# Kernel tuning notes

Hardware: AMD Instinct MI355X
Metric: run time of the kernel (lower is better)

The kernel has to match this reference:

```python
import jax, jax.numpy as jnp
import numpy as np


def setup_inputs() -> dict:
    key = jax.random.key(0)
    ks = jax.random.split(key, 4)
    T, B, E = 2048, 2, 1024
    query = jax.random.normal(ks[0], (T, B, E), dtype=jnp.float32)
    attn_mask = jnp.zeros((T, T), dtype=jnp.float32)
    Wqkv = jax.random.normal(ks[1], (3 * E, E), dtype=jnp.float32) * 0.02
    bqkv = jnp.zeros((3 * E,), dtype=jnp.float32)
    Wout = jax.random.normal(ks[2], (E, E), dtype=jnp.float32) * 0.02
    bout = jnp.zeros((E,), dtype=jnp.float32)
    return {"query": query, "attn_mask": attn_mask, "Wqkv": Wqkv,
            "bqkv": bqkv, "Wout": Wout, "bout": bout, "num_heads": 16}


def reference(query, attn_mask, Wqkv, bqkv, Wout, bout, num_heads):
    T, B, E = query.shape
    H = num_heads
    hd = E // H
    scaling = hd ** -0.5
    # fused QKV projection: [T,B,3E]
    qkv = jnp.einsum('tbe,fe->tbf', query, Wqkv) + bqkv
    q, k, v = jnp.split(qkv, 3, axis=-1)
    q = q * scaling
    # [T,B,E] -> [B*H, T, hd]
    def to_heads(x):
        return x.reshape(T, B * H, hd).transpose(1, 0, 2)
    q, k, v = to_heads(q), to_heads(k), to_heads(v)
    # scores [B*H, T, T]
    scores = jnp.einsum('bth,bsh->bts', q, k) + attn_mask[None, :, :]
    probs = jax.nn.softmax(scores, axis=-1)  # dropout p=0
    attn = jnp.einsum('bts,bsh->bth', probs, v)  # [B*H, T, hd]
    attn = attn.transpose(1, 0, 2).reshape(T, B, E)
    out = jnp.einsum('tbe,fe->tbf', attn, Wout) + bout
    avg_w = probs.reshape(B, H, T, T).sum(axis=1) / H
    return out, avg_w
```

## Files before the change

kernel.cpp:

```cpp
#include <hip/hip_runtime.h>
#include <cstdint>
#include <cstddef>

#define Tt 2048
#define Bb 2
#define Ee 1024
#define Hh 16
#define HD 64
#define BHh (Bb*Hh)
#define Mm (Tt*Bb)

typedef short bf16x8 __attribute__((ext_vector_type(8)));
typedef float f32x4  __attribute__((ext_vector_type(4)));

#define MFMA16(a,b,c) __builtin_amdgcn_mfma_f32_16x16x32_bf16(a, b, c, 0, 0, 0)

__device__ __forceinline__ unsigned short f2bf(float f) {
    unsigned int u = __builtin_bit_cast(unsigned int, f);
    u += 0x7FFFu + ((u >> 16) & 1u);
    return (unsigned short)(u >> 16);
}
__device__ __forceinline__ unsigned int pack2bf(float lo, float hi) {
    return (unsigned int)f2bf(lo) | ((unsigned int)f2bf(hi) << 16);
}

__device__ __forceinline__ bf16x8 ldfrag(const unsigned short* base, int row, int col) {
    const unsigned int* p = (const unsigned int*)(base + row*66 + col);
    const unsigned int* q = (const unsigned int*)(base + row*66 + col + 16);
    uint4 u;
    u.x = p[0]; u.y = p[1];
    u.z = q[0]; u.w = q[1];
    return __builtin_bit_cast(bf16x8, u);
}

__global__ __launch_bounds__(256)
void to_bf16(const float* __restrict__ src, unsigned short* __restrict__ dst, int n8)
{
    const int stride = gridDim.x * 256;
    for (int i = blockIdx.x*256 + threadIdx.x; i < n8; i += stride) {
        const float4 a = ((const float4*)src)[2*i];
        const float4 b = ((const float4*)src)[2*i + 1];
        const uint4 u = {pack2bf(a.x,a.y), pack2bf(a.z,a.w),
                         pack2bf(b.x,b.y), pack2bf(b.z,b.w)};
        ((uint4*)dst)[i] = u;
    }
}

template<int MODE>
__global__ __launch_bounds__(256)
void gemm_mfma(const unsigned short* __restrict__ A, const unsigned short* __restrict__ W,
               const float* __restrict__ bias, float* __restrict__ Cout,
               unsigned short* __restrict__ qbuf, unsigned short* __restrict__ kbuf,
               unsigned short* __restrict__ vbuf, int N, int K)
{
    __shared__ unsigned short As[128][66];
    __shared__ unsigned short Ws[128][66];
    const int tid  = threadIdx.x;
    const int bm   = blockIdx.y * 128;
    const int bn   = blockIdx.x * 128;
    const int w    = tid >> 6;
    const int lane = tid & 63;
    const int lr   = lane & 15;
    const int lg   = lane >> 4;
    const int wm   = (w >> 1) * 64;
    const int wn   = (w & 1) * 64;

    f32x4 acc[4][4];
#pragma unroll
    for (int m = 0; m < 4; ++m)
#pragma unroll
        for (int n = 0; n < 4; ++n)
            acc[m][n] = f32x4{0.f, 0.f, 0.f, 0.f};

    const int sr = tid >> 1;
    const int sc = (tid & 1) * 16;

    for (int k0 = 0; k0 < K; k0 += 32) {
        __syncthreads();
        {
            const unsigned short* Ap = &A[(size_t)(bm + sr) * K + k0 + sc];
            const unsigned short* Wp = &W[(size_t)(bn + sr) * K + k0 + sc];
            const uint4 a0 = *(const uint4*)Ap;
            const uint4 a1 = *(const uint4*)(Ap + 8);
            const uint4 w0 = *(const uint4*)Wp;
            const uint4 w1 = *(const uint4*)(Wp + 8);
            *(uint4*)&As[sr][sc]     = a0;
            *(uint4*)&As[sr][sc + 8] = a1;
            *(uint4*)&Ws[sr][sc]     = w0;
            *(uint4*)&Ws[sr][sc + 8] = w1;
        }
        __syncthreads();

        bf16x8 af[4], wf[4];
#pragma unroll
        for (int i = 0; i < 4; ++i) {
            af[i] = ldfrag(&As[0][0], wm + 16*i + lr, 4*lg);
            wf[i] = ldfrag(&Ws[0][0], wn + 16*i + lr, 4*lg);
        }
#pragma unroll
        for (int m = 0; m < 4; ++m)
#pragma unroll
            for (int n = 0; n < 4; ++n)
                acc[m][n] = MFMA16(af[m], wf[n], acc[m][n]);
    }

#pragma unroll
    for (int nsub = 0; nsub < 4; ++nsub) {
        const int n0 = bn + wn + 16*nsub + lr;
        const float bv = bias[n0];
#pragma unroll
        for (int msub = 0; msub < 4; ++msub) {
#pragma unroll
            for (int reg = 0; reg < 4; ++reg) {
                const int m = bm + wm + 16*msub + 4*lg + reg;
                float v = acc[msub][nsub][reg] + bv;
                if (MODE == 0) {
                    const int which = n0 >> 10;
                    const int e0 = n0 & 1023;
                    const int h = e0 >> 6, d0 = e0 & 63;
                    if (which == 0) v *= 0.125f;
                    unsigned short* dst = (which == 0) ? qbuf : (which == 1) ? kbuf : vbuf;
                    dst[((size_t)((m & 1)*Hh + h) * Tt + (m >> 1)) * HD + d0] = f2bf(v);
                } else {
                    Cout[(size_t)m * N + n0] = v;
                }
            }
        }
    }
}

__global__ __launch_bounds__(512)
void attn_mfma(const unsigned short* __restrict__ qb, const unsigned short* __restrict__ kb,
               const unsigned short* __restrict__ vb, const float* __restrict__ mask,
               unsigned short* __restrict__ attnb, float* __restrict__ lbuf)
{
    __shared__ unsigned short Ks[64][66];
    __shared__ unsigned short Vt[64][66];
    __shared__ float l_sh[128];

    const int tid  = threadIdx.x;
    const int bid  = blockIdx.x;
    const int wid  = (bid & 7) * 64 + (bid >> 3);
    const int bh   = wid & 31;
    const int t0   = (wid >> 5) * 128;
    const int w    = tid >> 6;
    const int lane = tid & 63;
    const int lr   = lane & 15;
    const int lg   = lane >> 4;
    const int b = bh >> 4, h = bh & 15;

    const unsigned short* __restrict__ Qg = qb + (size_t)bh * Tt * HD;
    const unsigned short* __restrict__ Kg = kb + (size_t)bh * Tt * HD;
    const unsigned short* __restrict__ Vg = vb + (size_t)bh * Tt * HD;

    const int str = tid >> 3;
    const int stc = (tid & 7) * 8;

    bf16x8 qf[2];
    for (int half = 0; half < 2; ++half) {
        __syncthreads();
        *(uint4*)&Ks[str][stc] =
            *(const uint4*)&Qg[(size_t)(t0 + half*64 + str) * HD + stc];
        __syncthreads();
        if ((w >> 2) == half) {
            const int r = 16*(w & 3) + lr;
            qf[0] = ldfrag(&Ks[0][0], r, 4*lg);
            qf[1] = ldfrag(&Ks[0][0], r, 32 + 4*lg);
        }
    }

    f32x4 oacc[4];
#pragma unroll
    for (int d = 0; d < 4; ++d)
        oacc[d] = f32x4{0.f, 0.f, 0.f, 0.f};
    float lacc = 0.f;

    for (int s0 = 0; s0 < Tt; s0 += 64) {
        __syncthreads();
        *(uint4*)&Ks[str][stc] =
            *(const uint4*)&Kg[(size_t)(s0 + str) * HD + stc];
        {
            const int dg = tid & 15, s2 = tid >> 4;
            const uint2 a = *(const uint2*)&Vg[(size_t)(s0 + 2*s2)     * HD + dg*4];
            const uint2 c = *(const uint2*)&Vg[(size_t)(s0 + 2*s2 + 1) * HD + dg*4];
            *(unsigned int*)&Vt[dg*4+0][2*s2] = (a.x & 0xFFFFu) | (c.x << 16);
            *(unsigned int*)&Vt[dg*4+1][2*s2] = (a.x >> 16)     | (c.x & 0xFFFF0000u);
            *(unsigned int*)&Vt[dg*4+2][2*s2] = (a.y & 0xFFFFu) | (c.y << 16);
            *(unsigned int*)&Vt[dg*4+3][2*s2] = (a.y >> 16)     | (c.y & 0xFFFF0000u);
        }
        __syncthreads();

        f32x4 sacc[4];
#pragma unroll
        for (int ssub = 0; ssub < 4; ++ssub) {
            const bf16x8 a0 = ldfrag(&Ks[0][0], 16*ssub + lr, 4*lg);
            const bf16x8 a1 = ldfrag(&Ks[0][0], 16*ssub + lr, 32 + 4*lg);
            f32x4 z = {0.f, 0.f, 0.f, 0.f};
            z = MFMA16(a0, qf[0], z);
            z = MFMA16(a1, qf[1], z);
            sacc[ssub] = z;
        }

        unsigned int pw[8];
        {
            float lt = 0.f;
            const float* __restrict__ mrow =
                &mask[(size_t)(t0 + 16*w + lr) * Tt + s0];
#pragma unroll
            for (int ssub = 0; ssub < 4; ++ssub) {
                const float4 mv = *(const float4*)&mrow[16*ssub + 4*lg];
                const float e0 = __expf(sacc[ssub][0] + mv.x);
                const float e1 = __expf(sacc[ssub][1] + mv.y);
                const float e2 = __expf(sacc[ssub][2] + mv.z);
                const float e3 = __expf(sacc[ssub][3] + mv.w);
                lt += (e0 + e1) + (e2 + e3);
                pw[ssub*2]     = pack2bf(e0, e1);
                pw[ssub*2 + 1] = pack2bf(e2, e3);
            }
            lt += __shfl_xor(lt, 16);
            lt += __shfl_xor(lt, 32);
            lacc += lt;
        }

        const uint4 ua = {pw[0], pw[1], pw[2], pw[3]};
        const uint4 ub = {pw[4], pw[5], pw[6], pw[7]};
#pragma unroll
        for (int dsub = 0; dsub < 4; ++dsub) {
            const bf16x8 b0 = ldfrag(&Vt[0][0], 16*dsub + lr, 4*lg);
            const bf16x8 b1 = ldfrag(&Vt[0][0], 16*dsub + lr, 32 + 4*lg);
            oacc[dsub] = MFMA16(__builtin_bit_cast(bf16x8, ua), b0, oacc[dsub]);
            oacc[dsub] = MFMA16(__builtin_bit_cast(bf16x8, ub), b1, oacc[dsub]);
        }
    }

    __syncthreads();
    if (lg == 0) l_sh[16*w + lr] = lacc;
    __syncthreads();
#pragma unroll
    for (int reg = 0; reg < 4; ++reg) {
        const int tl = 16*w + 4*lg + reg;
        const float inv = 1.f / l_sh[tl];
        const int t = t0 + tl;
#pragma unroll
        for (int dsub = 0; dsub < 4; ++dsub)
            attnb[((size_t)t * Bb + b) * Ee + h*HD + dsub*16 + lr] =
                f2bf(oacc[dsub][reg] * inv);
    }
    if (lg == 0)
        lbuf[(size_t)bh * Tt + t0 + 16*w + lr] = lacc;
}

__global__ __launch_bounds__(256)
void avg_probs_mfma(const unsigned short* __restrict__ qb, const unsigned short* __restrict__ kb,
                    const float* __restrict__ mask, const float* __restrict__ lbuf,
                    float* __restrict__ avg)
{
    __shared__ unsigned short Qs[64][66];
    __shared__ unsigned short Ksh[64][66];
    __shared__ float linv[16][64];

    const int tid  = threadIdx.x;
    const int b    = blockIdx.z;
    const int t0   = blockIdx.y * 64;
    const int s0   = blockIdx.x * 64;
    const int w    = tid >> 6;
    const int lane = tid & 63;
    const int lr   = lane & 15;
    const int lg   = lane >> 4;

    {
        const int h = tid >> 4, tl = (tid & 15) * 4;
        const float4 lv = *(const float4*)&lbuf[(size_t)(b*Hh + h) * Tt + t0 + tl];
        linv[h][tl+0] = 1.f / (16.f * lv.x);
        linv[h][tl+1] = 1.f / (16.f * lv.y);
        linv[h][tl+2] = 1.f / (16.f * lv.z);
        linv[h][tl+3] = 1.f / (16.f * lv.w);
    }

    f32x4 mf[4];
#pragma unroll
    for (int ssub = 0; ssub < 4; ++ssub)
#pragma unroll
        for (int reg = 0; reg < 4; ++reg)
            mf[ssub][reg] = mask[(size_t)(t0 + 16*w + 4*lg + reg) * Tt + s0 + 16*ssub + lr];

    f32x4 av[4];
#pragma unroll
    for (int ssub = 0; ssub < 4; ++ssub) av[ssub] = f32x4{0.f, 0.f, 0.f, 0.f};

    const int str = tid >> 2;
    const int stc = (tid & 3) * 16;

    for (int h = 0; h < Hh; ++h) {
        const unsigned short* __restrict__ Qg = qb + (size_t)(b*Hh + h) * Tt * HD;
        const unsigned short* __restrict__ Kg = kb + (size_t)(b*Hh + h) * Tt * HD;
        __syncthreads();
        {
            const unsigned short* Qp = &Qg[(size_t)(t0 + str) * HD + stc];
            const unsigned short* Kp = &Kg[(size_t)(s0 + str) * HD + stc];
            const uint4 q0 = *(const uint4*)Qp;
            const uint4 q1 = *(const uint4*)(Qp + 8);
            const uint4 k0 = *(const uint4*)Kp;
            const uint4 k1 = *(const uint4*)(Kp + 8);
            *(uint4*)&Qs[str][stc]      = q0;
            *(uint4*)&Qs[str][stc + 8]  = q1;
            *(uint4*)&Ksh[str][stc]     = k0;
            *(uint4*)&Ksh[str][stc + 8] = k1;
        }
        __syncthreads();

        const float lv0 = linv[h][16*w + 4*lg + 0];
        const float lv1 = linv[h][16*w + 4*lg + 1];
        const float lv2 = linv[h][16*w + 4*lg + 2];
        const float lv3 = linv[h][16*w + 4*lg + 3];

        const bf16x8 af0 = ldfrag(&Qs[0][0], 16*w + lr, 4*lg);
        const bf16x8 af1 = ldfrag(&Qs[0][0], 16*w + lr, 32 + 4*lg);
#pragma unroll
        for (int ssub = 0; ssub < 4; ++ssub) {
            const bf16x8 bf0 = ldfrag(&Ksh[0][0], 16*ssub + lr, 4*lg);
            const bf16x8 bf1 = ldfrag(&Ksh[0][0], 16*ssub + lr, 32 + 4*lg);
            f32x4 z = {0.f, 0.f, 0.f, 0.f};
            z = MFMA16(af0, bf0, z);
            z = MFMA16(af1, bf1, z);
            av[ssub][0] += __expf(z[0] + mf[ssub][0]) * lv0;
            av[ssub][1] += __expf(z[1] + mf[ssub][1]) * lv1;
            av[ssub][2] += __expf(z[2] + mf[ssub][2]) * lv2;
            av[ssub][3] += __expf(z[3] + mf[ssub][3]) * lv3;
        }
    }

#pragma unroll
    for (int ssub = 0; ssub < 4; ++ssub)
#pragma unroll
        for (int reg = 0; reg < 4; ++reg)
            avg[((size_t)b * Tt + t0 + 16*w + 4*lg + reg) * Tt + s0 + 16*ssub + lr] =
                av[ssub][reg];
}

extern "C" void kernel_launch(void* const* d_in, const int* in_sizes, int n_in,
                              void* d_out, int out_size, void* d_ws, size_t ws_size,
                              hipStream_t stream)
{
    (void)in_sizes; (void)n_in; (void)out_size; (void)ws_size;
    const float* query = (const float*)d_in[0];
    const float* mask  = (const float*)d_in[1];
    const float* Wqkv  = (const float*)d_in[2];
    const float* bqkv  = (const float*)d_in[3];
    const float* Wout  = (const float*)d_in[4];
    const float* bout  = (const float*)d_in[5];

    float* out = (float*)d_out;
    float* avg = out + (size_t)Tt * Bb * Ee;

    const size_t S1 = (size_t)BHh * Tt * HD;
    unsigned short* wsu     = (unsigned short*)d_ws;
    unsigned short* qbuf    = wsu;
    unsigned short* kbuf    = qbuf + S1;
    unsigned short* vbuf    = kbuf + S1;
    unsigned short* attnb   = vbuf + S1;
    unsigned short* querybf = attnb + (size_t)Mm * Ee;
    unsigned short* wqkvbf  = querybf + (size_t)Mm * Ee;
    unsigned short* woutbf  = wqkvbf + (size_t)3 * Ee * Ee;
    float*          lbuf    = (float*)(woutbf + (size_t)Ee * Ee);

    to_bf16<<<1024, 256, 0, stream>>>(query, querybf, (Mm*Ee)/8);
    to_bf16<<<1024, 256, 0, stream>>>(Wqkv, wqkvbf, (3*Ee*Ee)/8);
    to_bf16<<<512,  256, 0, stream>>>(Wout, woutbf, (Ee*Ee)/8);

    gemm_mfma<0><<<dim3(3072/128, Mm/128), 256, 0, stream>>>(
        querybf, wqkvbf, bqkv, nullptr, qbuf, kbuf, vbuf, 3072, Ee);
    attn_mfma<<<dim3(BHh * (Tt/128)), 512, 0, stream>>>(
        qbuf, kbuf, vbuf, mask, attnb, lbuf);
    avg_probs_mfma<<<dim3(Tt/64, Tt/64, Bb), 256, 0, stream>>>(
        qbuf, kbuf, mask, lbuf, avg);
    gemm_mfma<1><<<dim3(Ee/128, Mm/128), 256, 0, stream>>>(
        attnb, woutbf, bout, out, nullptr, nullptr, nullptr, Ee, Ee);
}
```

Baseline: 244.3 us.

## Use XOR-swizzled LDS layouts with 128-bit fragment loads in GEMM and attention

Replaces the padded (stride-66) shared-memory tiles with unpadded dword arrays indexed through XOR swizzles, in both the projection GEMM and the attention kernel. Fragments are now read with single 128-bit LDS loads instead of four 32-bit loads. The V transpose store is remapped with a permuted column index so the MFMA k-ordering stays consistent between the P and V operands. The aim is fewer LDS instructions and fewer bank conflicts, at the cost of trickier indexing that must keep the QK and PV contraction orderings matched.

```diff
diff --git a/kernel.cpp b/kernel.cpp
--- a/kernel.cpp
+++ b/kernel.cpp
@@ -24,6 +24,13 @@
     return (unsigned int)f2bf(lo) | ((unsigned int)f2bf(hi) << 16);
 }
 
+__device__ __forceinline__ int swzA(int row, int dwcol) {
+    return (row*32 + dwcol) ^ ((row & 7) << 2);
+}
+__device__ __forceinline__ int swzG(int row, int dwcol) {
+    return (row*16 + dwcol) ^ ((row & 3) << 2);
+}
+
 __device__ __forceinline__ bf16x8 ldfrag(const unsigned short* base, int row, int col) {
     const unsigned int* p = (const unsigned int*)(base + row*66 + col);
     const unsigned int* q = (const unsigned int*)(base + row*66 + col + 16);
@@ -53,8 +60,8 @@
                unsigned short* __restrict__ qbuf, unsigned short* __restrict__ kbuf,
                unsigned short* __restrict__ vbuf, int N, int K)
 {
-    __shared__ unsigned short As[128][66];
-    __shared__ unsigned short Ws[128][66];
+    __shared__ __align__(16) unsigned int AsDW[128*16];
+    __shared__ __align__(16) unsigned int WsDW[128*16];
     const int tid  = threadIdx.x;
     const int bm   = blockIdx.y * 128;
     const int bn   = blockIdx.x * 128;
@@ -72,30 +79,28 @@
         for (int n = 0; n < 4; ++n)
             acc[m][n] = f32x4{0.f, 0.f, 0.f, 0.f};
 
-    const int sr = tid >> 1;
-    const int sc = (tid & 1) * 16;
+    const int r1  = tid >> 2;
+    const int cdw = (tid & 3) * 4;
 
     for (int k0 = 0; k0 < K; k0 += 32) {
         __syncthreads();
         {
-            const unsigned short* Ap = &A[(size_t)(bm + sr) * K + k0 + sc];
-            const unsigned short* Wp = &W[(size_t)(bn + sr) * K + k0 + sc];
-            const uint4 a0 = *(const uint4*)Ap;
-            const uint4 a1 = *(const uint4*)(Ap + 8);
-            const uint4 w0 = *(const uint4*)Wp;
-            const uint4 w1 = *(const uint4*)(Wp + 8);
-            *(uint4*)&As[sr][sc]     = a0;
-            *(uint4*)&As[sr][sc + 8] = a1;
-            *(uint4*)&Ws[sr][sc]     = w0;
-            *(uint4*)&Ws[sr][sc + 8] = w1;
+            const uint4 a0 = *(const uint4*)&A[(size_t)(bm + r1)      * K + k0 + cdw*2];
+            const uint4 a1 = *(const uint4*)&A[(size_t)(bm + r1 + 64) * K + k0 + cdw*2];
+            const uint4 w0 = *(const uint4*)&W[(size_t)(bn + r1)      * K + k0 + cdw*2];
+            const uint4 w1 = *(const uint4*)&W[(size_t)(bn + r1 + 64) * K + k0 + cdw*2];
+            *(uint4*)(AsDW + swzG(r1,      cdw)) = a0;
+            *(uint4*)(AsDW + swzG(r1 + 64, cdw)) = a1;
+            *(uint4*)(WsDW + swzG(r1,      cdw)) = w0;
+            *(uint4*)(WsDW + swzG(r1 + 64, cdw)) = w1;
         }
         __syncthreads();
 
         bf16x8 af[4], wf[4];
 #pragma unroll
         for (int i = 0; i < 4; ++i) {
-            af[i] = ldfrag(&As[0][0], wm + 16*i + lr, 4*lg);
-            wf[i] = ldfrag(&Ws[0][0], wn + 16*i + lr, 4*lg);
+            af[i] = __builtin_bit_cast(bf16x8, *(const uint4*)(AsDW + swzG(wm + 16*i + lr, 4*lg)));
+            wf[i] = __builtin_bit_cast(bf16x8, *(const uint4*)(WsDW + swzG(wn + 16*i + lr, 4*lg)));
         }
 #pragma unroll
         for (int m = 0; m < 4; ++m)
@@ -134,8 +139,8 @@
                const unsigned short* __restrict__ vb, const float* __restrict__ mask,
                unsigned short* __restrict__ attnb, float* __restrict__ lbuf)
 {
-    __shared__ unsigned short Ks[64][66];
-    __shared__ unsigned short Vt[64][66];
+    __shared__ __align__(16) unsigned int KsDW[64*32];
+    __shared__ __align__(16) unsigned int VtDW[64*32];
     __shared__ float l_sh[128];
 
     const int tid  = threadIdx.x;
@@ -154,18 +159,23 @@
     const unsigned short* __restrict__ Vg = vb + (size_t)bh * Tt * HD;
 
     const int str = tid >> 3;
-    const int stc = (tid & 7) * 8;
+    const int sdw = (tid & 7) * 4;
+
+    const int vs  = 2 * (tid & 31);
+    const int vdg = tid >> 5;
+    const int pc_dw = (((vs & 3) | (((vs >> 4) & 1) << 2) |
+                        (((vs >> 2) & 3) << 3) | ((vs >> 5) << 5))) >> 1;
 
     bf16x8 qf[2];
     for (int half = 0; half < 2; ++half) {
         __syncthreads();
-        *(uint4*)&Ks[str][stc] =
-            *(const uint4*)&Qg[(size_t)(t0 + half*64 + str) * HD + stc];
+        *(uint4*)(KsDW + swzA(str, sdw)) =
+            *(const uint4*)&Qg[(size_t)(t0 + half*64 + str) * HD + sdw*2];
         __syncthreads();
         if ((w >> 2) == half) {
             const int r = 16*(w & 3) + lr;
-            qf[0] = ldfrag(&Ks[0][0], r, 4*lg);
-            qf[1] = ldfrag(&Ks[0][0], r, 32 + 4*lg);
+            qf[0] = __builtin_bit_cast(bf16x8, *(const uint4*)(KsDW + swzA(r, 4*lg)));
+            qf[1] = __builtin_bit_cast(bf16x8, *(const uint4*)(KsDW + swzA(r, 16 + 4*lg)));
         }
     }
 
@@ -177,24 +187,25 @@
 
     for (int s0 = 0; s0 < Tt; s0 += 64) {
         __syncthreads();
-        *(uint4*)&Ks[str][stc] =
-            *(const uint4*)&Kg[(size_t)(s0 + str) * HD + stc];
+        *(uint4*)(KsDW + swzA(str, sdw)) =
+            *(const uint4*)&Kg[(size_t)(s0 + str) * HD + sdw*2];
         {
-            const int dg = tid & 15, s2 = tid >> 4;
-            const uint2 a = *(const uint2*)&Vg[(size_t)(s0 + 2*s2)     * HD + dg*4];
-            const uint2 c = *(const uint2*)&Vg[(size_t)(s0 + 2*s2 + 1) * HD + dg*4];
-            *(unsigned int*)&Vt[dg*4+0][2*s2] = (a.x & 0xFFFFu) | (c.x << 16);
-            *(unsigned int*)&Vt[dg*4+1][2*s2] = (a.x >> 16)     | (c.x & 0xFFFF0000u);
-            *(unsigned int*)&Vt[dg*4+2][2*s2] = (a.y & 0xFFFFu) | (c.y << 16);
-            *(unsigned int*)&Vt[dg*4+3][2*s2] = (a.y >> 16)     | (c.y & 0xFFFF0000u);
+            const uint2 a = *(const uint2*)&Vg[(size_t)(s0 + vs)     * HD + vdg*4];
+            const uint2 c = *(const uint2*)&Vg[(size_t)(s0 + vs + 1) * HD + vdg*4];
+            VtDW[swzA(vdg*4+0, pc_dw)] = (a.x & 0xFFFFu) | (c.x << 16);
+            VtDW[swzA(vdg*4+1, pc_dw)] = (a.x >> 16)     | (c.x & 0xFFFF0000u);
+            VtDW[swzA(vdg*4+2, pc_dw)] = (a.y & 0xFFFFu) | (c.y << 16);
+            VtDW[swzA(vdg*4+3, pc_dw)] = (a.y >> 16)     | (c.y & 0xFFFF0000u);
         }
         __syncthreads();
 
         f32x4 sacc[4];
 #pragma unroll
         for (int ssub = 0; ssub < 4; ++ssub) {
-            const bf16x8 a0 = ldfrag(&Ks[0][0], 16*ssub + lr, 4*lg);
-            const bf16x8 a1 = ldfrag(&Ks[0][0], 16*ssub + lr, 32 + 4*lg);
+            const bf16x8 a0 = __builtin_bit_cast(bf16x8,
+                *(const uint4*)(KsDW + swzA(16*ssub + lr, 4*lg)));
+            const bf16x8 a1 = __builtin_bit_cast(bf16x8,
+                *(const uint4*)(KsDW + swzA(16*ssub + lr, 16 + 4*lg)));
             f32x4 z = {0.f, 0.f, 0.f, 0.f};
             z = MFMA16(a0, qf[0], z);
             z = MFMA16(a1, qf[1], z);
@@ -226,8 +237,10 @@
         const uint4 ub = {pw[4], pw[5], pw[6], pw[7]};
 #pragma unroll
         for (int dsub = 0; dsub < 4; ++dsub) {
-            const bf16x8 b0 = ldfrag(&Vt[0][0], 16*dsub + lr, 4*lg);
-            const bf16x8 b1 = ldfrag(&Vt[0][0], 16*dsub + lr, 32 + 4*lg);
+            const bf16x8 b0 = __builtin_bit_cast(bf16x8,
+                *(const uint4*)(VtDW + swzA(16*dsub + lr, 4*lg)));
+            const bf16x8 b1 = __builtin_bit_cast(bf16x8,
+                *(const uint4*)(VtDW + swzA(16*dsub + lr, 16 + 4*lg)));
             oacc[dsub] = MFMA16(__builtin_bit_cast(bf16x8, ua), b0, oacc[dsub]);
             oacc[dsub] = MFMA16(__builtin_bit_cast(bf16x8, ub), b1, oacc[dsub]);
         }
```

Result: no change. 246.3 us (+0.8%).
